# Kernel tuning notes

Hardware: AMD Instinct MI355X
Metric: run time of the kernel (lower is better)

The kernel has to match this reference:

```python
import jax, jax.numpy as jnp
import numpy as np

T, H, I, E, TOPK = 2048, 2048, 1408, 8, 2


def setup_inputs() -> dict:
    key = jax.random.key(0)
    k1, k2, k3, k4 = jax.random.split(key, 4)
    x = jax.random.normal(k1, (T, H), dtype=jnp.float32)
    router_logits = jax.random.normal(k2, (T, E), dtype=jnp.float32)
    # scale weights down so activations stay well-conditioned
    w13_weight = jax.random.normal(k3, (E, 2 * I, H), dtype=jnp.float32) * (1.0 / np.sqrt(H))
    w2_weight = jax.random.normal(k4, (E, H, I), dtype=jnp.float32) * (1.0 / np.sqrt(I))
    return {"x": x, "router_logits": router_logits, "w13_weight": w13_weight,
            "w2_weight": w2_weight, "top_k": TOPK}


def reference(x, router_logits, w13_weight, w2_weight, top_k):
    # --- select_experts: softmax scoring, top-k, renormalize ---
    probs = jax.nn.softmax(router_logits.astype(jnp.float32), axis=-1)   # [T, E]
    topk_w, topk_ids = jax.lax.top_k(probs, top_k)                        # [T, k]
    topk_w = topk_w / jnp.sum(topk_w, axis=-1, keepdims=True)             # renormalize
    topk_w = topk_w.astype(x.dtype)

    n_tok = x.shape[0]
    n_exp = w13_weight.shape[0]
    inter = w2_weight.shape[2]

    # dense combine weights [T, E]: zero for unselected experts
    comb = jnp.zeros((n_tok, n_exp), dtype=x.dtype)
    comb = comb.at[jnp.arange(n_tok)[:, None], topk_ids].add(topk_w)

    # --- fused_experts: gated SiLU MLP per expert, weighted combine ---
    gate_up = jnp.einsum('th,eih->tei', x, w13_weight)                    # [T, E, 2I]
    gate, up = gate_up[..., :inter], gate_up[..., inter:]
    act = jax.nn.silu(gate) * up                                          # [T, E, I]
    out = jnp.einsum('tei,ehi,te->th', act, w2_weight, comb)              # [T, H]
    return out
```

## Files before the change

### kernel.cpp

```cpp
#include <hip/hip_runtime.h>
#include <hip/hip_bf16.h>
#include <stdint.h>

#define T_TOK 2048
#define H_DIM 2048
#define I_DIM 1408
#define NEXP  8
#define NPOS  4096
#define NPAD  5120
#define MAXT  40

typedef short short8 __attribute__((ext_vector_type(8)));
typedef float f32x4  __attribute__((ext_vector_type(4)));

__device__ __forceinline__ short f2bf(float f) {
  union { float f; uint32_t u; } v; v.f = f;
  uint32_t r = (v.u + 0x7FFFu + ((v.u >> 16) & 1u)) >> 16;
  return (short)r;
}
__device__ __forceinline__ float bf2f(short s) {
  union { uint32_t u; float f; } v; v.u = ((uint32_t)(uint16_t)s) << 16;
  return v.f;
}

__device__ __forceinline__ short8 cvt8(f32x4 a, f32x4 b) {
  __hip_bfloat162 h0 = __float22bfloat162_rn(float2{a[0], a[1]});
  __hip_bfloat162 h1 = __float22bfloat162_rn(float2{a[2], a[3]});
  __hip_bfloat162 h2 = __float22bfloat162_rn(float2{b[0], b[1]});
  __hip_bfloat162 h3 = __float22bfloat162_rn(float2{b[2], b[3]});
  short2 s0, s1, s2, s3;
  __builtin_memcpy(&s0, &h0, 4); __builtin_memcpy(&s1, &h1, 4);
  __builtin_memcpy(&s2, &h2, 4); __builtin_memcpy(&s3, &h3, 4);
  short8 r;
  r[0] = s0.x; r[1] = s0.y; r[2] = s1.x; r[3] = s1.y;
  r[4] = s2.x; r[5] = s2.y; r[6] = s3.x; r[7] = s3.y;
  return r;
}

__device__ __forceinline__ void load_lds16(const void* g, void* l) {
  __builtin_amdgcn_global_load_lds((const __attribute__((address_space(1))) uint32_t*)g,
                                   (__attribute__((address_space(3))) uint32_t*)l,
                                   16, 0, 0);
}

__global__ void k_routing(const float* __restrict__ logits,
                          int* __restrict__ pos_token,
                          float* __restrict__ pos_w,
                          int* __restrict__ eoff,
                          int* __restrict__ inv) {
  __shared__ int   s_ids[T_TOK];
  __shared__ float s_w0[T_TOK];
  __shared__ float s_w1[T_TOK];
  __shared__ int s_cnt[NEXP], s_cur[NEXP], s_off[NEXP + 1];
  const int tid = threadIdx.x;
  if (tid < NEXP) { s_cnt[tid] = 0; s_cur[tid] = 0; }
  for (int p = tid; p < NPAD; p += blockDim.x) { pos_token[p] = 0; pos_w[p] = 0.f; }
  __syncthreads();

  for (int t = tid; t < T_TOK; t += blockDim.x) {
    float l[NEXP];
#pragma unroll
    for (int e = 0; e < NEXP; ++e) l[e] = logits[t * NEXP + e];
    int b0 = 0; float v0 = l[0];
#pragma unroll
    for (int e = 1; e < NEXP; ++e) if (l[e] > v0) { v0 = l[e]; b0 = e; }
    int b1 = -1; float v1 = -1e30f;
#pragma unroll
    for (int e = 0; e < NEXP; ++e) if (e != b0 && l[e] > v1) { v1 = l[e]; b1 = e; }
    float t1 = __expf(v1 - v0);
    float w0 = 1.f / (1.f + t1);
    float w1 = 1.f - w0;
    s_ids[t] = b0 | (b1 << 8);
    s_w0[t] = w0; s_w1[t] = w1;
    atomicAdd(&s_cnt[b0], 1);
    atomicAdd(&s_cnt[b1], 1);
  }
  __syncthreads();
  if (tid == 0) {
    int acc = 0;
    for (int e = 0; e < NEXP; ++e) {
      s_off[e] = acc;
      acc += (s_cnt[e] + 127) & ~127;
    }
    s_off[NEXP] = acc;
    for (int e = 0; e <= NEXP; ++e) eoff[e] = s_off[e];
  }
  __syncthreads();
  for (int t = tid; t < T_TOK; t += blockDim.x) {
    int ids = s_ids[t];
    int e0 = ids & 255, e1 = ids >> 8;
    int p0 = s_off[e0] + atomicAdd(&s_cur[e0], 1);
    pos_token[p0] = t; pos_w[p0] = s_w0[t];
    int p1 = s_off[e1] + atomicAdd(&s_cur[e1], 1);
    pos_token[p1] = t; pos_w[p1] = s_w1[t];
    inv[2 * t] = p0; inv[2 * t + 1] = p1;
  }
}

__global__ void k_gather(const float* __restrict__ x,
                         const int* __restrict__ pos_token,
                         short* __restrict__ xg) {
  const int p = blockIdx.x;
  const int tid = threadIdx.x;
  const int tok = pos_token[p];
  const f32x4* src = (const f32x4*)(x + (size_t)tok * H_DIM);
  f32x4 a = src[tid * 2];
  f32x4 b = src[tid * 2 + 1];
  ((short8*)(xg + (size_t)p * H_DIM))[tid] = cvt8(a, b);
}

__device__ __forceinline__ int tile_expert(const int* eoff, int row0) {
  int e = 0;
#pragma unroll
  for (int i = 1; i < NEXP; ++i) if (row0 >= eoff[i]) e = i;
  return e;
}

__global__ __launch_bounds__(256, 3) void k_gateup(
    const short* __restrict__ xg, const float* __restrict__ w13,
    const int* __restrict__ eoff, short* __restrict__ act) {
  __shared__ __align__(16) short a_s[2][128 * 32];
  __shared__ __align__(16) short bg_s[2][64 * 32];
  __shared__ __align__(16) short bu_s[2][64 * 32];

  const int bxr = blockIdx.x;
  const int chunk = bxr & 7;
  const int local = bxr >> 3;
  const int nt = local / 5;
  const int tile = chunk * 5 + (local % 5);
  const int row0 = tile * 128;
  if (row0 >= eoff[NEXP]) return;
  const int e = tile_expert(eoff, row0);

  const int tid = threadIdx.x;
  const int wid = tid >> 6;
  const int lane = tid & 63;
  const int wm = wid >> 1, wn = wid & 1;

  f32x4 accg[4][2] = {};
  f32x4 accu[4][2] = {};

  const short* aG  = xg + (size_t)row0 * H_DIM;
  const float* bgG = w13 + (size_t)e * (2 * I_DIM) * H_DIM + (size_t)(nt * 64) * H_DIM;
  const float* buG = bgG + (size_t)I_DIM * H_DIM;

  const int row  = tid >> 2;
  const int scol = ((tid & 3) ^ ((tid >> 3) & 3)) * 8;

  auto stageA = [&](int t, int bi) {
    const int ks = t * 32;
    load_lds16(aG + (size_t)row * H_DIM + ks + scol,        (char*)a_s[bi] + wid * 1024);
    load_lds16(aG + (size_t)(64 + row) * H_DIM + ks + scol, (char*)a_s[bi] + 4096 + wid * 1024);
  };

  f32x4 g0, g1, u0, u1;
  auto ldB = [&](int t) {
    const int ks = t * 32;
    const float* sg = bgG + (size_t)row * H_DIM + ks + scol;
    const float* su = buG + (size_t)row * H_DIM + ks + scol;
    g0 = *(const f32x4*)sg; g1 = *(const f32x4*)(sg + 4);
    u0 = *(const f32x4*)su; u1 = *(const f32x4*)(su + 4);
  };
  auto wrB = [&](int bi) {
    *(short8*)((char*)bg_s[bi] + tid * 16) = cvt8(g0, g1);
    *(short8*)((char*)bu_s[bi] + tid * 16) = cvt8(u0, u1);
  };

  auto compute = [&](int bi) {
    const int asl = ((lane >> 4) ^ ((lane >> 1) & 3)) * 16;
    short8 af[4];
#pragma unroll
    for (int fm = 0; fm < 4; ++fm) {
      int m = wm * 64 + fm * 16 + (lane & 15);
      af[fm] = *(const short8*)((const char*)a_s[bi] + m * 64 + asl);
    }
#pragma unroll
    for (int fn = 0; fn < 2; ++fn) {
      int n = wn * 32 + fn * 16 + (lane & 15);
      short8 bg = *(const short8*)((const char*)bg_s[bi] + n * 64 + asl);
      short8 bu = *(const short8*)((const char*)bu_s[bi] + n * 64 + asl);
#pragma unroll
      for (int fm = 0; fm < 4; ++fm)
        accg[fm][fn] = __builtin_amdgcn_mfma_f32_16x16x32_bf16(af[fm], bg, accg[fm][fn], 0, 0, 0);
#pragma unroll
      for (int fm = 0; fm < 4; ++fm)
        accu[fm][fn] = __builtin_amdgcn_mfma_f32_16x16x32_bf16(af[fm], bu, accu[fm][fn], 0, 0, 0);
    }
  };

  const int NK = H_DIM / 32;
  stageA(0, 0); ldB(0); wrB(0);
  __syncthreads();
  for (int t = 0; t < NK; ++t) {
    int bi = t & 1;
    if (t + 1 < NK) { stageA(t + 1, bi ^ 1); ldB(t + 1); }
    compute(bi);
    if (t + 1 < NK) wrB(bi ^ 1);
    __syncthreads();
  }

#pragma unroll
  for (int fm = 0; fm < 4; ++fm) {
#pragma unroll
    for (int rr = 0; rr < 4; ++rr) {
      int m = wm * 64 + fm * 16 + (lane >> 4) * 4 + rr;
      size_t grow = (size_t)(row0 + m);
#pragma unroll
      for (int fn = 0; fn < 2; ++fn) {
        int col = nt * 64 + wn * 32 + fn * 16 + (lane & 15);
        float g = accg[fm][fn][rr];
        float u = accu[fm][fn][rr];
        float a = g / (1.f + __expf(-g)) * u;
        act[grow * I_DIM + col] = f2bf(a);
      }
    }
  }
}

__global__ __launch_bounds__(256, 3) void k_down(
    const short* __restrict__ act, const float* __restrict__ w2,
    const int* __restrict__ eoff, short* __restrict__ y) {
  __shared__ __align__(16) short a_s[2][128 * 32];
  __shared__ __align__(16) short b_s[2][128 * 32];

  int bxr = blockIdx.x;
  const int bx = (bxr & 7) * 80 + (bxr >> 3);
  const int tile = bx >> 4;
  const int nt = bx & 15;
  const int row0 = tile * 128;
  if (row0 >= eoff[NEXP]) return;
  const int e = tile_expert(eoff, row0);

  const int tid = threadIdx.x;
  const int wid = tid >> 6;
  const int lane = tid & 63;
  const int wm = wid >> 1, wn = wid & 1;

  f32x4 acc[4][4] = {};

  const short* aG = act + (size_t)row0 * I_DIM;
  const float* bG = w2 + (size_t)e * H_DIM * I_DIM + (size_t)(nt * 128) * I_DIM;

  const int row  = tid >> 2;
  const int scol = ((tid & 3) ^ ((tid >> 3) & 3)) * 8;

  auto stageA = [&](int t, int bi) {
    const int ks = t * 32;
    load_lds16(aG + (size_t)row * I_DIM + ks + scol,        (char*)a_s[bi] + wid * 1024);
    load_lds16(aG + (size_t)(64 + row) * I_DIM + ks + scol, (char*)a_s[bi] + 4096 + wid * 1024);
  };
  auto ldB = [&](int t, f32x4& b00, f32x4& b01, f32x4& b10, f32x4& b11) {
    const int ks = t * 32;
    const float* s0 = bG + (size_t)row * I_DIM + ks + scol;
    const float* s1 = bG + (size_t)(64 + row) * I_DIM + ks + scol;
    b00 = *(const f32x4*)s0; b01 = *(const f32x4*)(s0 + 4);
    b10 = *(const f32x4*)s1; b11 = *(const f32x4*)(s1 + 4);
  };
  auto wrB = [&](int bi, f32x4& b00, f32x4& b01, f32x4& b10, f32x4& b11) {
    *(short8*)((char*)b_s[bi] + tid * 16)        = cvt8(b00, b01);
    *(short8*)((char*)b_s[bi] + 4096 + tid * 16) = cvt8(b10, b11);
  };

  auto compute = [&](int bi) {
    const int asl = ((lane >> 4) ^ ((lane >> 1) & 3)) * 16;
    short8 af[4];
#pragma unroll
    for (int fm = 0; fm < 4; ++fm) {
      int m = wm * 64 + fm * 16 + (lane & 15);
      af[fm] = *(const short8*)((const char*)a_s[bi] + m * 64 + asl);
    }
#pragma unroll
    for (int fn = 0; fn < 4; ++fn) {
      int n = wn * 64 + fn * 16 + (lane & 15);
      short8 bb = *(const short8*)((const char*)b_s[bi] + n * 64 + asl);
#pragma unroll
      for (int fm = 0; fm < 4; ++fm)
        acc[fm][fn] = __builtin_amdgcn_mfma_f32_16x16x32_bf16(af[fm], bb, acc[fm][fn], 0, 0, 0);
    }
  };

  const int NK = I_DIM / 32;
  f32x4 e0, e1, e2, e3, o0, o1, o2, o3;

  stageA(0, 0);
  ldB(0, e0, e1, e2, e3);
  wrB(0, e0, e1, e2, e3);
  ldB(1, e0, e1, e2, e3);
  ldB(2, o0, o1, o2, o3);
  __syncthreads();

#define DN_STEP(T, B0, B1, B2, B3)                                            \
  {                                                                           \
    const int t_ = (T);                                                       \
    const int bi_ = t_ & 1;                                                   \
    const int tn_ = (t_ + 1 < NK) ? t_ + 1 : NK - 1;                          \
    const int tf_ = (t_ + 3 < NK) ? t_ + 3 : NK - 1;                          \
    stageA(tn_, bi_ ^ 1);                                                     \
    __builtin_amdgcn_sched_barrier(0);                                        \
    wrB(bi_ ^ 1, B0, B1, B2, B3);                                             \
    ldB(tf_, B0, B1, B2, B3);                                                 \
    compute(bi_);                                                             \
    asm volatile("s_waitcnt vmcnt(4) lgkmcnt(0)" ::: "memory");               \
    __builtin_amdgcn_s_barrier();                                             \
  }
  for (int tp = 0; tp < NK; tp += 2) {
    DN_STEP(tp,     e0, e1, e2, e3);
    DN_STEP(tp + 1, o0, o1, o2, o3);
  }
#undef DN_STEP
  asm volatile("s_waitcnt vmcnt(0)" ::: "memory");

#pragma unroll
  for (int fm = 0; fm < 4; ++fm) {
#pragma unroll
    for (int rr = 0; rr < 4; ++rr) {
      int m = wm * 64 + fm * 16 + (lane >> 4) * 4 + rr;
      size_t grow = (size_t)(row0 + m);
#pragma unroll
      for (int fn = 0; fn < 4; ++fn) {
        int col = nt * 128 + wn * 64 + fn * 16 + (lane & 15);
        y[grow * H_DIM + col] = f2bf(acc[fm][fn][rr]);
      }
    }
  }
}

__global__ void k_combine(const short* __restrict__ y,
                          const int* __restrict__ inv,
                          const float* __restrict__ pos_w,
                          float* __restrict__ out) {
  const int t = blockIdx.x;
  const int tid = threadIdx.x;
  const int p0 = inv[2 * t], p1 = inv[2 * t + 1];
  const float w0 = pos_w[p0], w1 = pos_w[p1];
  short8 a = ((const short8*)(y + (size_t)p0 * H_DIM))[tid];
  short8 b = ((const short8*)(y + (size_t)p1 * H_DIM))[tid];
  f32x4 r0, r1;
#pragma unroll
  for (int j = 0; j < 4; ++j) {
    r0[j] = w0 * bf2f(a[j]) + w1 * bf2f(b[j]);
    r1[j] = w0 * bf2f(a[j + 4]) + w1 * bf2f(b[j + 4]);
  }
  f32x4* o = (f32x4*)(out + (size_t)t * H_DIM);
  o[tid * 2]     = r0;
  o[tid * 2 + 1] = r1;
}

extern "C" void kernel_launch(void* const* d_in, const int* in_sizes, int n_in,
                              void* d_out, int out_size, void* d_ws, size_t ws_size,
                              hipStream_t stream) {
  const float* x      = (const float*)d_in[0];
  const float* logits = (const float*)d_in[1];
  const float* w13    = (const float*)d_in[2];
  const float* w2     = (const float*)d_in[3];
  (void)in_sizes; (void)n_in; (void)out_size; (void)ws_size;
  float* out = (float*)d_out;
  char* ws = (char*)d_ws;

  size_t o = 0;
  auto alloc = [&](size_t bytes) { size_t r = o; o += (bytes + 255) & ~(size_t)255; return r; };
  short* xg        = (short*)(ws + alloc((size_t)NPAD * H_DIM * 2));
  short* act       = (short*)(ws + alloc((size_t)NPAD * I_DIM * 2));
  short* y         = (short*)(ws + alloc((size_t)NPAD * H_DIM * 2));
  int*   pos_token = (int*)  (ws + alloc((size_t)NPAD * 4));
  float* pos_w     = (float*)(ws + alloc((size_t)NPAD * 4));
  int*   inv       = (int*)  (ws + alloc((size_t)T_TOK * 2 * 4));
  int*   eoff      = (int*)  (ws + alloc((NEXP + 1) * 4));

  k_routing<<<1, 1024, 0, stream>>>(logits, pos_token, pos_w, eoff, inv);
  k_gather<<<NPAD, 256, 0, stream>>>(x, pos_token, xg);
  k_gateup<<<MAXT * 22, 256, 0, stream>>>(xg, w13, eoff, act);
  k_down<<<MAXT * 16, 256, 0, stream>>>(act, w2, eoff, y);
  k_combine<<<T_TOK, 256, 0, stream>>>(y, inv, pos_w, out);
}
```

Baseline: 216.5 us.

## Restructure gate-up GEMM to one block per expert and N-tile with tall M tiles

The gate/up kernel now launches one 512-thread block per (expert, 64-column tile) and loops over that expert's rows in 640-row chunks. Each fp32 weight tile is read and converted to bf16 once per expert chunk rather than once per 128-row tile, which cuts redundant weight traffic and conversion work. The cost is a grid of only 176 blocks with heavy per-block LDS use, so the device may be under-occupied and work may be unevenly spread when experts receive different token counts.

```diff
diff --git a/kernel.cpp b/kernel.cpp
--- a/kernel.cpp
+++ b/kernel.cpp
@@ -5,6 +5,7 @@
 #define T_TOK 2048
 #define H_DIM 2048
 #define I_DIM 1408
+#define GU_W  2816
 #define NEXP  8
 #define NPOS  4096
 #define NPAD  5120
@@ -116,102 +117,107 @@
   return e;
 }
 
-__global__ __launch_bounds__(256, 3) void k_gateup(
+__global__ __launch_bounds__(512, 1) void k_gateup(
     const short* __restrict__ xg, const float* __restrict__ w13,
     const int* __restrict__ eoff, short* __restrict__ act) {
-  __shared__ __align__(16) short a_s[2][128 * 32];
+  __shared__ __align__(16) short a_s[2][640 * 32];
   __shared__ __align__(16) short bg_s[2][64 * 32];
   __shared__ __align__(16) short bu_s[2][64 * 32];
 
   const int bxr = blockIdx.x;
-  const int chunk = bxr & 7;
-  const int local = bxr >> 3;
-  const int nt = local / 5;
-  const int tile = chunk * 5 + (local % 5);
-  const int row0 = tile * 128;
-  if (row0 >= eoff[NEXP]) return;
-  const int e = tile_expert(eoff, row0);
+  const int e = bxr & 7;
+  const int nt = bxr >> 3;
+  const int off = eoff[e], end = eoff[e + 1];
 
   const int tid = threadIdx.x;
   const int wid = tid >> 6;
   const int lane = tid & 63;
-  const int wm = wid >> 1, wn = wid & 1;
-
-  f32x4 accg[4][2] = {};
-  f32x4 accu[4][2] = {};
-
-  const short* aG  = xg + (size_t)row0 * H_DIM;
-  const float* bgG = w13 + (size_t)e * (2 * I_DIM) * H_DIM + (size_t)(nt * 64) * H_DIM;
+
+  const float* bgG = w13 + (size_t)e * GU_W * H_DIM + (size_t)(nt * 64) * H_DIM;
   const float* buG = bgG + (size_t)I_DIM * H_DIM;
 
-  const int row  = tid >> 2;
+  const int arow = tid >> 2;
   const int scol = ((tid & 3) ^ ((tid >> 3) & 3)) * 8;
-
-  auto stageA = [&](int t, int bi) {
-    const int ks = t * 32;
-    load_lds16(aG + (size_t)row * H_DIM + ks + scol,        (char*)a_s[bi] + wid * 1024);
-    load_lds16(aG + (size_t)(64 + row) * H_DIM + ks + scol, (char*)a_s[bi] + 4096 + wid * 1024);
-  };
-
-  f32x4 g0, g1, u0, u1;
-  auto ldB = [&](int t) {
-    const int ks = t * 32;
-    const float* sg = bgG + (size_t)row * H_DIM + ks + scol;
-    const float* su = buG + (size_t)row * H_DIM + ks + scol;
-    g0 = *(const f32x4*)sg; g1 = *(const f32x4*)(sg + 4);
-    u0 = *(const f32x4*)su; u1 = *(const f32x4*)(su + 4);
-  };
-  auto wrB = [&](int bi) {
-    *(short8*)((char*)bg_s[bi] + tid * 16) = cvt8(g0, g1);
-    *(short8*)((char*)bu_s[bi] + tid * 16) = cvt8(u0, u1);
-  };
-
-  auto compute = [&](int bi) {
-    const int asl = ((lane >> 4) ^ ((lane >> 1) & 3)) * 16;
-    short8 af[4];
-#pragma unroll
-    for (int fm = 0; fm < 4; ++fm) {
-      int m = wm * 64 + fm * 16 + (lane & 15);
-      af[fm] = *(const short8*)((const char*)a_s[bi] + m * 64 + asl);
-    }
-#pragma unroll
-    for (int fn = 0; fn < 2; ++fn) {
-      int n = wn * 32 + fn * 16 + (lane & 15);
-      short8 bg = *(const short8*)((const char*)bg_s[bi] + n * 64 + asl);
-      short8 bu = *(const short8*)((const char*)bu_s[bi] + n * 64 + asl);
-#pragma unroll
-      for (int fm = 0; fm < 4; ++fm)
-        accg[fm][fn] = __builtin_amdgcn_mfma_f32_16x16x32_bf16(af[fm], bg, accg[fm][fn], 0, 0, 0);
-#pragma unroll
-      for (int fm = 0; fm < 4; ++fm)
-        accu[fm][fn] = __builtin_amdgcn_mfma_f32_16x16x32_bf16(af[fm], bu, accu[fm][fn], 0, 0, 0);
-    }
-  };
-
-  const int NK = H_DIM / 32;
-  stageA(0, 0); ldB(0); wrB(0);
-  __syncthreads();
-  for (int t = 0; t < NK; ++t) {
-    int bi = t & 1;
-    if (t + 1 < NK) { stageA(t + 1, bi ^ 1); ldB(t + 1); }
-    compute(bi);
-    if (t + 1 < NK) wrB(bi ^ 1);
+  const int t2 = tid & 255;
+  const int brow = t2 >> 2;
+  const int bscol = ((t2 & 3) ^ ((t2 >> 3) & 3)) * 8;
+  const float* bHalf = (tid < 256) ? bgG : buG;
+
+  for (int base = off; base < end; base += 640) {
+    f32x4 accg[5][4] = {};
+    f32x4 accu[5][4] = {};
+
+    auto stageA = [&](int t, int bi) {
+      const int ks = t * 32;
+#pragma unroll
+      for (int r = 0; r < 5; ++r) {
+        int gr = base + r * 128 + arow;
+        if (gr > NPAD - 1) gr = NPAD - 1;
+        load_lds16(xg + (size_t)gr * H_DIM + ks + scol,
+                   (char*)a_s[bi] + r * 8192 + wid * 1024);
+      }
+    };
+
+    f32x4 b0, b1;
+    auto ldB = [&](int t) {
+      const int ks = t * 32;
+      const float* s = bHalf + (size_t)brow * H_DIM + ks + bscol;
+      b0 = *(const f32x4*)s; b1 = *(const f32x4*)(s + 4);
+    };
+    auto wrB = [&](int bi) {
+      char* d = (tid < 256) ? (char*)bg_s[bi] : (char*)bu_s[bi];
+      *(short8*)(d + t2 * 16) = cvt8(b0, b1);
+    };
+
+    auto compute = [&](int bi) {
+      const int asl = ((lane >> 4) ^ ((lane >> 1) & 3)) * 16;
+      short8 af[5];
+#pragma unroll
+      for (int fm = 0; fm < 5; ++fm) {
+        int m = wid * 80 + fm * 16 + (lane & 15);
+        af[fm] = *(const short8*)((const char*)a_s[bi] + m * 64 + asl);
+      }
+#pragma unroll
+      for (int fn = 0; fn < 4; ++fn) {
+        int n = fn * 16 + (lane & 15);
+        short8 bg = *(const short8*)((const char*)bg_s[bi] + n * 64 + asl);
+        short8 bu = *(const short8*)((const char*)bu_s[bi] + n * 64 + asl);
+#pragma unroll
+        for (int fm = 0; fm < 5; ++fm)
+          accg[fm][fn] = __builtin_amdgcn_mfma_f32_16x16x32_bf16(af[fm], bg, accg[fm][fn], 0, 0, 0);
+#pragma unroll
+        for (int fm = 0; fm < 5; ++fm)
+          accu[fm][fn] = __builtin_amdgcn_mfma_f32_16x16x32_bf16(af[fm], bu, accu[fm][fn], 0, 0, 0);
+      }
+    };
+
+    const int NK = H_DIM / 32;
+    stageA(0, 0); ldB(0); wrB(0);
     __syncthreads();
-  }
-
-#pragma unroll
-  for (int fm = 0; fm < 4; ++fm) {
-#pragma unroll
-    for (int rr = 0; rr < 4; ++rr) {
-      int m = wm * 64 + fm * 16 + (lane >> 4) * 4 + rr;
-      size_t grow = (size_t)(row0 + m);
-#pragma unroll
-      for (int fn = 0; fn < 2; ++fn) {
-        int col = nt * 64 + wn * 32 + fn * 16 + (lane & 15);
-        float g = accg[fm][fn][rr];
-        float u = accu[fm][fn][rr];
-        float a = g / (1.f + __expf(-g)) * u;
-        act[grow * I_DIM + col] = f2bf(a);
+    for (int t = 0; t < NK; ++t) {
+      int bi = t & 1;
+      if (t + 1 < NK) { stageA(t + 1, bi ^ 1); ldB(t + 1); }
+      compute(bi);
+      if (t + 1 < NK) wrB(bi ^ 1);
+      __syncthreads();
+    }
+
+#pragma unroll
+    for (int fm = 0; fm < 5; ++fm) {
+#pragma unroll
+      for (int rr = 0; rr < 4; ++rr) {
+        int m = wid * 80 + fm * 16 + (lane >> 4) * 4 + rr;
+        int grow = base + m;
+        if (grow < end) {
+#pragma unroll
+          for (int fn = 0; fn < 4; ++fn) {
+            int col = nt * 64 + fn * 16 + (lane & 15);
+            float g = accg[fm][fn][rr];
+            float u = accu[fm][fn][rr];
+            float a = g / (1.f + __expf(-g)) * u;
+            act[(size_t)grow * I_DIM + col] = f2bf(a);
+          }
+        }
       }
     }
   }
@@ -369,7 +375,7 @@
 
   k_routing<<<1, 1024, 0, stream>>>(logits, pos_token, pos_w, eoff, inv);
   k_gather<<<NPAD, 256, 0, stream>>>(x, pos_token, xg);
-  k_gateup<<<MAXT * 22, 256, 0, stream>>>(xg, w13, eoff, act);
+  k_gateup<<<NEXP * 22, 512, 0, stream>>>(xg, w13, eoff, act);
   k_down<<<MAXT * 16, 256, 0, stream>>>(act, w2, eoff, y);
   k_combine<<<T_TOK, 256, 0, stream>>>(y, inv, pos_w, out);
 }
```

Result: no change. 212.8 us (-1.7%).
